# Performance work log

Measured on AMD Instinct MI355X. Metric: run time of the kernel, lower is better.

The kernel has to match this reference:

```python
import jax, jax.numpy as jnp
import numpy as np

M, NQ, NKV = 8, 256, 4096
E, H, D = 1024, 16, 64  # embed_dim, num_heads, head_dim
SCALE = D ** -0.5


def setup_inputs() -> dict:
    key = jax.random.key(0)
    ks = jax.random.split(key, 6)
    zq = jax.random.normal(ks[0], (M, NQ, E), dtype=jnp.float32)
    zkv = jax.random.normal(ks[1], (M, NKV, E), dtype=jnp.float32)
    xq = jax.random.normal(ks[2], (M, NQ, E), dtype=jnp.float32)
    xkv = jax.random.normal(ks[3], (M, NKV, E), dtype=jnp.float32)
    Wq = jax.random.normal(ks[4], (E, H * D), dtype=jnp.float32) / np.sqrt(E)
    Wk = jax.random.normal(ks[5], (E, H * D), dtype=jnp.float32) / np.sqrt(E)
    raw_head_weights = jnp.ones((H,), dtype=jnp.float32)
    return {"zq": zq, "zkv": zkv, "xq": xq, "xkv": xkv,
            "Wq": Wq, "Wk": Wk, "raw_head_weights": raw_head_weights}


def reference(zq, zkv, xq, xkv, Wq, Wk, raw_head_weights):
    # project + split heads: [m, h, n, d]
    q = jnp.einsum('mne,ehd->mhnd', zq, Wq.reshape(E, H, D))
    k = jnp.einsum('mne,ehd->mhnd', zkv, Wk.reshape(E, H, D))
    # SDPA with V = xkv broadcast across heads
    scores = jnp.einsum('mhqd,mhkd->mhqk', q, k) * SCALE
    attn = jax.nn.softmax(scores, axis=-1)
    # attn @ V with broadcast V [m, nkv, dx] -> per-head outputs [m, h, nq, dx]
    out = jnp.einsum('mhqk,mkd->mhqd', attn, xkv)
    # head-weighted combine + residual
    head_weights = jax.nn.softmax(raw_head_weights, axis=0)
    xq_update = jnp.einsum('mhqd,h->mqd', out, head_weights)
    xq_out = xq + xq_update
    return (zq, xq_out)
```

## Files before the change

### kernel.cpp

```cpp
#include <hip/hip_runtime.h>
#include <hip/hip_bf16.h>
#include <stdint.h>

#define MB_  8
#define NQ_  256
#define NKV_ 4096
#define E_   1024
#define H_   16
#define D_   64

typedef __bf16 bf16x8 __attribute__((ext_vector_type(8)));
typedef float  f32x4  __attribute__((ext_vector_type(4)));
typedef unsigned short u16;
typedef unsigned short u16x8 __attribute__((ext_vector_type(8)));

#define MFMA16(a,b,c) __builtin_amdgcn_mfma_f32_16x16x32_bf16((a),(b),(c),0,0,0)

__device__ __forceinline__ u16 f2bf(float f) {
  uint32_t u = __float_as_uint(f);
  u += 0x7fffu + ((u >> 16) & 1u);
  return (u16)(u >> 16);
}

__device__ __forceinline__ u16x8 pack8(f32x4 a, f32x4 b) {
  u16x8 v;
  v[0] = f2bf(a[0]); v[1] = f2bf(a[1]); v[2] = f2bf(a[2]); v[3] = f2bf(a[3]);
  v[4] = f2bf(b[0]); v[5] = f2bf(b[1]); v[6] = f2bf(b[2]); v[7] = f2bf(b[3]);
  return v;
}

__device__ __forceinline__ void gload_lds16(const void* g, void* l) {
  __builtin_amdgcn_global_load_lds(
      (const __attribute__((address_space(1))) void*)g,
      (__attribute__((address_space(3))) void*)l, 16, 0, 0);
}

__device__ __forceinline__ void stage_tile(const char* __restrict__ g, int ldbytes,
                                           char* lds, int t) {
  int srcCB = (((t & 7) ^ ((t >> 3) & 7)) << 4);
  const char* gp = g + (long long)(t >> 3) * ldbytes + srcCB;
  char* lp = lds + ((t >> 6) << 10);
#pragma unroll
  for (int i = 0; i < 4; ++i) {
    gload_lds16(gp + (long long)(32 * i) * ldbytes, lp + i * 4096);
  }
}

__device__ __forceinline__ bf16x8 read_frag(const char* lds, int r, int cb) {
  return *(const bf16x8*)(lds + r * 128 + (cb ^ ((r & 7) << 4)));
}

template <int MODE>
__global__ __launch_bounds__(256, 2) void gemm_nt(
    const u16* __restrict__ A, const u16* __restrict__ Bt, void* __restrict__ Cv,
    int lda, int ldb, int ldc, int K,
    long long sA, long long sB, long long sC) {
  __shared__ __align__(16) char smA[16384];
  __shared__ __align__(16) char smB[16384];
  int zz = blockIdx.z;
  int b = (MODE == 2) ? (zz & 7) : zz;
  int ks = (MODE == 2) ? (zz >> 3) : 0;
  long long koff = (long long)ks * 1024;

  unsigned nwg = gridDim.x * gridDim.y;
  unsigned orig = blockIdx.y * gridDim.x + blockIdx.x;
  unsigned cpx = nwg >> 3;
  unsigned swz = (orig & 7) * cpx + (orig >> 3);
  unsigned bx = swz % gridDim.x, by = swz / gridDim.x;

  const char* Ap = (const char*)(A + (long long)b * sA + (long long)by * 128 * lda + koff);
  const char* Bp = (const char*)(Bt + (long long)b * sB + (long long)bx * 128 * ldb + koff);

  int t = threadIdx.x, lane = t & 63;
  int wm = t >> 7, wn = (t >> 6) & 1;
  int rl = lane & 15, kq = lane >> 4;

  f32x4 acc[4][4];
#pragma unroll
  for (int i = 0; i < 4; ++i)
#pragma unroll
    for (int j = 0; j < 4; ++j) acc[i][j] = (f32x4){0.f, 0.f, 0.f, 0.f};

  int ldab = lda * 2, ldbb = ldb * 2;
  for (int k0 = 0; k0 < K; k0 += 64) {
    stage_tile(Ap + k0 * 2, ldab, smA, t);
    stage_tile(Bp + k0 * 2, ldbb, smB, t);
    __syncthreads();
    bf16x8 af[4][2], bf[4][2];
#pragma unroll
    for (int f = 0; f < 4; ++f)
#pragma unroll
      for (int ksl = 0; ksl < 2; ++ksl) {
        af[f][ksl] = read_frag(smA, wm * 64 + f * 16 + rl, ksl * 64 + kq * 16);
        bf[f][ksl] = read_frag(smB, wn * 64 + f * 16 + rl, ksl * 64 + kq * 16);
      }
#pragma unroll
    for (int fm = 0; fm < 4; ++fm)
#pragma unroll
      for (int fn = 0; fn < 4; ++fn) {
        acc[fm][fn] = MFMA16(af[fm][0], bf[fn][0], acc[fm][fn]);
        acc[fm][fn] = MFMA16(af[fm][1], bf[fn][1], acc[fm][fn]);
      }
    __syncthreads();
  }

#pragma unroll
  for (int fm = 0; fm < 4; ++fm)
#pragma unroll
    for (int fn = 0; fn < 4; ++fn)
#pragma unroll
      for (int j = 0; j < 4; ++j) {
        int row = by * 128 + wm * 64 + fm * 16 + kq * 4 + j;
        int col = bx * 128 + wn * 64 + fn * 16 + rl;
        if (MODE == 0) {
          ((u16*)Cv)[(long long)b * sC + (long long)row * ldc + col] = f2bf(acc[fm][fn][j]);
        } else {
          float* dst = (float*)Cv + ((long long)(ks * 8 + b)) * sC +
                       (long long)row * ldc + col;
          __builtin_nontemporal_store(acc[fm][fn][j], dst);
        }
      }
}

__device__ __forceinline__ void stage32(const char* __restrict__ g, int ldbytes,
                                        char* ldsbuf, int t, long long koffB) {
  int w = t >> 6, lane = t & 63;
#pragma unroll
  for (int i = 0; i < 2; ++i) {
    int c = w + i * 8;
    int slot = c * 64 + lane;
    int row = slot >> 2, c16 = slot & 3;
    int srcc = (c16 ^ ((row >> 1) & 3)) << 4;
    gload_lds16(g + (long long)row * ldbytes + koffB + srcc,
                ldsbuf + c * 1024);
  }
}

__device__ __forceinline__ bf16x8 frag32(const char* ldsbuf, int r, int kq) {
  return *(const bf16x8*)(ldsbuf + r * 64 + ((kq ^ ((r >> 1) & 3)) << 4));
}

__global__ __launch_bounds__(512, 2) void gemm256(
    const u16* __restrict__ A, const u16* __restrict__ Bt, u16* __restrict__ C,
    int lda, int ldb, int ldc, int K) {
  extern __shared__ char lds[];

  unsigned nwg = gridDim.x * gridDim.y;
  unsigned orig = blockIdx.y * gridDim.x + blockIdx.x;
  unsigned cpx = nwg >> 3;
  unsigned swz = (orig & 7) * cpx + (orig >> 3);
  unsigned bx = swz % gridDim.x, by = swz / gridDim.x;

  const char* Ap = (const char*)(A + (long long)by * 256 * lda);
  const char* Bp = (const char*)(Bt + (long long)bx * 256 * ldb);
  int ldab = lda * 2, ldbb = ldb * 2;

  int t = threadIdx.x, lane = t & 63;
  int wid = t >> 6, wm = wid >> 2, wn = wid & 3;
  int rl = lane & 15, kq = lane >> 4;

  f32x4 acc[8][4];
#pragma unroll
  for (int i = 0; i < 8; ++i)
#pragma unroll
    for (int j = 0; j < 4; ++j) acc[i][j] = (f32x4){0.f, 0.f, 0.f, 0.f};

  stage32(Ap, ldab, lds, t, 0);
  stage32(Bp, ldbb, lds + 16384, t, 0);
  stage32(Ap, ldab, lds + 32768, t, 64);
  stage32(Bp, ldbb, lds + 32768 + 16384, t, 64);
  asm volatile("s_waitcnt vmcnt(4)" ::: "memory");
  asm volatile("s_barrier" ::: "memory");

  int NT = K >> 5;
  for (int ts = 0; ts < NT; ++ts) {
    char* bufA = lds + (ts & 3) * 32768;
    char* bufB = bufA + 16384;
    if (ts + 2 < NT) {
      char* nb = lds + ((ts + 2) & 3) * 32768;
      stage32(Ap, ldab, nb, t, (long long)(ts + 2) << 6);
      stage32(Bp, ldbb, nb + 16384, t, (long long)(ts + 2) << 6);
    }
    bf16x8 af[8], bv[4];
#pragma unroll
    for (int fr = 0; fr < 8; ++fr) af[fr] = frag32(bufA, wm * 128 + fr * 16 + rl, kq);
#pragma unroll
    for (int fc = 0; fc < 4; ++fc) bv[fc] = frag32(bufB, wn * 64 + fc * 16 + rl, kq);
    __builtin_amdgcn_s_setprio(1);
#pragma unroll
    for (int fr = 0; fr < 8; ++fr)
#pragma unroll
      for (int fc = 0; fc < 4; ++fc)
        acc[fr][fc] = MFMA16(af[fr], bv[fc], acc[fr][fc]);
    __builtin_amdgcn_s_setprio(0);
    if (ts + 2 < NT)
      asm volatile("s_waitcnt vmcnt(4)" ::: "memory");
    else
      asm volatile("s_waitcnt vmcnt(0)" ::: "memory");
    asm volatile("s_barrier" ::: "memory");
  }

#pragma unroll
  for (int fr = 0; fr < 8; ++fr)
#pragma unroll
    for (int fc = 0; fc < 4; ++fc)
#pragma unroll
      for (int j = 0; j < 4; ++j) {
        int row = by * 256 + wm * 128 + fr * 16 + kq * 4 + j;
        int col = bx * 256 + wn * 64 + fc * 16 + rl;
        C[(long long)row * ldc + col] = f2bf(acc[fr][fc][j]);
      }
}

__global__ void pv_combine(const float* __restrict__ part, const float* __restrict__ xq,
                           float* __restrict__ out1) {
  int i = blockIdx.x * 256 + threadIdx.x;
  f32x4 s = __builtin_nontemporal_load((const f32x4*)xq + i);
#pragma unroll
  for (int k = 0; k < 4; ++k) {
    f32x4 p = __builtin_nontemporal_load((const f32x4*)(part + (long long)k * 2097152) + i);
    s += p;
  }
  ((f32x4*)out1)[i] = s;
}

__global__ __launch_bounds__(256, 4) void attn_stats(
    const u16* __restrict__ qg, const u16* __restrict__ kg,
    float* __restrict__ lstP) {
  __shared__ __align__(16) char smQ[16384];
  __shared__ __align__(16) char smK[16384];
  int kt = blockIdx.x, qt = blockIdx.y;
  int m = blockIdx.z >> 1, hh = blockIdx.z & 1;
  int t = threadIdx.x, lane = t & 63;
  int wm = t >> 7, wn = (t >> 6) & 1;
  int rl = lane & 15, kq = lane >> 4;

  const char* qbase = (const char*)(qg + ((long long)(m * NQ_ + qt * 128)) * 1024);
  const char* kbase = (const char*)(kg + ((long long)(m * NKV_ + kt * 128)) * 1024);

  for (int hi = 0; hi < 8; ++hi) {
    int h = hh * 8 + hi;
    stage_tile(qbase + h * 128, 2048, smQ, t);
    stage_tile(kbase + h * 128, 2048, smK, t);
    __syncthreads();
    bf16x8 kf[4][2], qf[4][2];
#pragma unroll
    for (int f = 0; f < 4; ++f)
#pragma unroll
      for (int ksl = 0; ksl < 2; ++ksl) {
        kf[f][ksl] = read_frag(smK, wm * 64 + f * 16 + rl, ksl * 64 + kq * 16);
        qf[f][ksl] = read_frag(smQ, wn * 64 + f * 16 + rl, ksl * 64 + kq * 16);
      }
    float rs[4] = {0.f, 0.f, 0.f, 0.f};
#pragma unroll
    for (int fm = 0; fm < 4; ++fm)
#pragma unroll
      for (int fn = 0; fn < 4; ++fn) {
        f32x4 sc = (f32x4){0.f, 0.f, 0.f, 0.f};
        sc = MFMA16(kf[fm][0], qf[fn][0], sc);
        sc = MFMA16(kf[fm][1], qf[fn][1], sc);
        rs[fn] += (__expf(sc[0]) + __expf(sc[1])) + (__expf(sc[2]) + __expf(sc[3]));
      }
#pragma unroll
    for (int fn = 0; fn < 4; ++fn) {
      float v = rs[fn];
      v += __shfl_xor(v, 16);
      v += __shfl_xor(v, 32);
      if (lane < 16) {
        int q = qt * 128 + wn * 64 + fn * 16 + rl;
        lstP[(long long)(kt * 2 + wm) * 32768 + ((m * H_ + h) << 8) + q] = v;
      }
    }
    __syncthreads();
  }
}

__global__ void stats_combine(const float* __restrict__ lp, float* __restrict__ lst) {
  int i = blockIdx.x * 256 + threadIdx.x;
  float s = 0.f;
#pragma unroll
  for (int k = 0; k < 64; ++k) s += lp[(long long)k * 32768 + i];
  lst[i] = s;
}

__global__ __launch_bounds__(256, 2) void pbar_kernel(
    const u16* __restrict__ qg, const u16* __restrict__ kg,
    const float* __restrict__ lstat,
    const float* __restrict__ rawhw, u16* __restrict__ Pbar) {
  __shared__ __align__(16) char smQ[16384];
  __shared__ __align__(16) char smK[16384];
  __shared__ float scf[2048];
  int kt = blockIdx.x, qt = blockIdx.y, m = blockIdx.z;
  int q0 = qt * 128, k0 = kt * 128;
  int t = threadIdx.x, lane = t & 63;
  int wm = t >> 7, wn = (t >> 6) & 1;
  int rl = lane & 15, kq = lane >> 4;

  float hm = -1e30f;
  for (int i = 0; i < H_; ++i) hm = fmaxf(hm, rawhw[i]);
  float hs = 0.f, hw[H_];
  for (int i = 0; i < H_; ++i) { hw[i] = __expf(rawhw[i] - hm); hs += hw[i]; }
  float hinv = 1.f / hs;
  for (int idx = t; idx < 2048; idx += 256) {
    int h = idx >> 7, r = idx & 127;
    scf[idx] = hw[h] * hinv / lstat[((m * H_ + h) << 8) + q0 + r];
  }

  f32x4 pacc[4][4];
#pragma unroll
  for (int i = 0; i < 4; ++i)
#pragma unroll
    for (int j = 0; j < 4; ++j) pacc[i][j] = (f32x4){0.f, 0.f, 0.f, 0.f};

  const char* qbase = (const char*)(qg + ((long long)(m * NQ_ + q0)) * 1024);
  const char* kbase = (const char*)(kg + ((long long)(m * NKV_ + k0)) * 1024);

  for (int h = 0; h < H_; ++h) {
    stage_tile(qbase + h * 128, 2048, smQ, t);
    stage_tile(kbase + h * 128, 2048, smK, t);
    __syncthreads();
    bf16x8 af[4][2], bfr[4][2];
#pragma unroll
    for (int f = 0; f < 4; ++f)
#pragma unroll
      for (int ksl = 0; ksl < 2; ++ksl) {
        af[f][ksl] = read_frag(smQ, wm * 64 + f * 16 + rl, ksl * 64 + kq * 16);
        bfr[f][ksl] = read_frag(smK, wn * 64 + f * 16 + rl, ksl * 64 + kq * 16);
      }
#pragma unroll
    for (int fm = 0; fm < 4; ++fm) {
      int rbase = wm * 64 + fm * 16 + kq * 4;
      float cf0 = scf[(h << 7) + rbase + 0];
      float cf1 = scf[(h << 7) + rbase + 1];
      float cf2 = scf[(h << 7) + rbase + 2];
      float cf3 = scf[(h << 7) + rbase + 3];
#pragma unroll
      for (int fn = 0; fn < 4; ++fn) {
        f32x4 sc = (f32x4){0.f, 0.f, 0.f, 0.f};
        sc = MFMA16(af[fm][0], bfr[fn][0], sc);
        sc = MFMA16(af[fm][1], bfr[fn][1], sc);
        pacc[fm][fn][0] += cf0 * __expf(sc[0]);
        pacc[fm][fn][1] += cf1 * __expf(sc[1]);
        pacc[fm][fn][2] += cf2 * __expf(sc[2]);
        pacc[fm][fn][3] += cf3 * __expf(sc[3]);
      }
    }
    __syncthreads();
  }
#pragma unroll
  for (int fm = 0; fm < 4; ++fm)
#pragma unroll
    for (int fn = 0; fn < 4; ++fn)
#pragma unroll
      for (int j = 0; j < 4; ++j) {
        int row = q0 + wm * 64 + fm * 16 + kq * 4 + j;
        int col = k0 + wn * 64 + fn * 16 + rl;
        Pbar[(((long long)m * NQ_ + row) << 12) + col] = f2bf(pacc[fm][fn][j]);
      }
}

__global__ void prep_kernel(const float* __restrict__ zq, u16* __restrict__ zqb,
                            float* __restrict__ out0,
                            const float* __restrict__ zkv, u16* __restrict__ zkvb,
                            const float* __restrict__ Wq, u16* __restrict__ WqT,
                            const float* __restrict__ Wk, u16* __restrict__ WkT,
                            const float* __restrict__ xkv, u16* __restrict__ xkvT) {
  __shared__ float tile[64][65];
  int bid = blockIdx.x;
  if (bid < 8704) {
    const float* in; u16* out; bool passthru; long long i;
    if (bid < 512) { in = zq; out = zqb; passthru = true; i = (long long)bid * 256 + threadIdx.x; }
    else { in = zkv; out = zkvb; passthru = false; i = (long long)(bid - 512) * 256 + threadIdx.x; }
    const f32x4* p = (const f32x4*)(in + i * 16);
    f32x4 a = __builtin_nontemporal_load(p);
    f32x4 b = __builtin_nontemporal_load(p + 1);
    f32x4 c = __builtin_nontemporal_load(p + 2);
    f32x4 d = __builtin_nontemporal_load(p + 3);
    if (passthru) {
      f32x4* o = (f32x4*)(out0 + i * 16);
      __builtin_nontemporal_store(a, o);
      __builtin_nontemporal_store(b, o + 1);
      __builtin_nontemporal_store(c, o + 2);
      __builtin_nontemporal_store(d, o + 3);
    }
    u16x8* q = (u16x8*)(out + i * 16);
    q[0] = pack8(a, b);
    q[1] = pack8(c, d);
    return;
  }
  const float* in; u16* out; int R, C; float alpha; int r0, c0; bool nts = false;
  if (bid < 8960) {
    int id = bid - 8704;
    in = Wq; out = WqT; R = 1024; C = 1024; alpha = 0.125f;
    r0 = (id & 15) * 64; c0 = (id >> 4) * 64;
  } else if (bid < 9216) {
    int id = bid - 8960;
    in = Wk; out = WkT; R = 1024; C = 1024; alpha = 1.0f;
    r0 = (id & 15) * 64; c0 = (id >> 4) * 64;
  } else {
    int id = bid - 9216;
    int bz = id >> 10, rem = id & 1023;
    in = xkv + (long long)bz * NKV_ * E_;
    out = xkvT + (long long)bz * NKV_ * E_;
    R = NKV_; C = E_; alpha = 1.0f;
    r0 = (rem & 63) * 64; c0 = (rem >> 6) * 64;
    nts = true;
  }
  int t = threadIdx.x;
  int rr = t >> 4, c4 = t & 15;
#pragma unroll
  for (int i = 0; i < 4; ++i) {
    f32x4 v = __builtin_nontemporal_load(
        (const f32x4*)(in + (long long)(r0 + rr + i * 16) * C + c0 + c4 * 4));
    float* d = &tile[rr + i * 16][c4 * 4];
    d[0] = v[0]; d[1] = v[1]; d[2] = v[2]; d[3] = v[3];
  }
  __syncthreads();
  int cc = t >> 3, r8 = t & 7;
#pragma unroll
  for (int i = 0; i < 2; ++i) {
    int c = cc + i * 32;
    u16x8 v;
#pragma unroll
    for (int j = 0; j < 8; ++j) v[j] = f2bf(alpha * tile[r8 * 8 + j][c]);
    u16x8* dst = (u16x8*)(out + (long long)(c0 + c) * R + r0 + r8 * 8);
    if (nts) __builtin_nontemporal_store(v, dst);
    else *dst = v;
  }
}

extern "C" void kernel_launch(void* const* d_in, const int* in_sizes, int n_in,
                              void* d_out, int out_size, void* d_ws, size_t ws_size,
                              hipStream_t stream) {
  const float* zq  = (const float*)d_in[0];
  const float* zkv = (const float*)d_in[1];
  const float* xq  = (const float*)d_in[2];
  const float* xkv = (const float*)d_in[3];
  const float* Wq  = (const float*)d_in[4];
  const float* Wk  = (const float*)d_in[5];
  const float* rhw = (const float*)d_in[6];
  float* out = (float*)d_out;

  char* ws = (char*)d_ws;
  u16* WqT  = (u16*)(ws);
  u16* WkT  = (u16*)(ws + (2ull << 20));
  u16* zqb  = (u16*)(ws + (4ull << 20));
  u16* qb   = (u16*)(ws + (8ull << 20));
  u16* kb   = (u16*)(ws + (12ull << 20));
  u16* xkvT = (u16*)(ws + (76ull << 20));
  char* zr  = ws + (140ull << 20);
  u16* zkvb = (u16*)zr;
  u16* Pbar = (u16*)zr;
  float* lst  = (float*)(zr + (18ull << 20));
  float* lstP = (float*)(zr + (20ull << 20));
  float* pvP  = (float*)(zr + (28ull << 20));

  (void)hipFuncSetAttribute((const void*)gemm256,
                            hipFuncAttributeMaxDynamicSharedMemorySize, 131072);

  prep_kernel<<<17408, 256, 0, stream>>>(zq, zqb, out, zkv, zkvb,
                                         Wq, WqT, Wk, WkT, xkv, xkvT);

  gemm_nt<0><<<dim3(8, 16, 1), 256, 0, stream>>>(zqb, WqT, qb,
                                                 1024, 1024, 1024, 1024, 0, 0, 0);
  gemm256<<<dim3(4, 128, 1), 512, 131072, stream>>>(zkvb, WkT, kb, 1024, 1024, 1024, 1024);

  attn_stats<<<dim3(32, 2, 16), 256, 0, stream>>>(qb, kb, lstP);
  stats_combine<<<128, 256, 0, stream>>>(lstP, lst);

  pbar_kernel<<<dim3(32, 2, 8), 256, 0, stream>>>(qb, kb, lst, rhw, Pbar);

  gemm_nt<2><<<dim3(8, 2, 32), 256, 0, stream>>>(Pbar, xkvT, pvP,
                                                 4096, 4096, 1024, 1024,
                                                 256LL * 4096, 1024LL * 4096,
                                                 256LL * 1024);
  pv_combine<<<2048, 256, 0, stream>>>(pvP, xq, out + (long long)MB_ * NQ_ * E_);
}
```

Before: 297.5 us.

## Double-buffer Q/K tiles in stats and Pbar kernels; fold log2e into Wq scale

attn_stats and pbar_kernel now ping-pong between two LDS buffers. Each iteration issues the direct-to-LDS loads for the next head before computing on the current one, with explicit vmcnt waits and raw s_barrier in place of __syncthreads. Separately, log2(e) is folded into the Wq prescale so the kernels can call exp2f instead of __expf, removing a multiply per exponential. The cost is twice the LDS (attn_stats launch bounds drop from 4 to 2 blocks per SM), and the hand-counted vmcnt values must match the number of loads stage_tile issues.

```diff
diff --git a/kernel.cpp b/kernel.cpp
--- a/kernel.cpp
+++ b/kernel.cpp
@@ -131,8 +131,7 @@
     int slot = c * 64 + lane;
     int row = slot >> 2, c16 = slot & 3;
     int srcc = (c16 ^ ((row >> 1) & 3)) << 4;
-    gload_lds16(g + (long long)row * ldbytes + koffB + srcc,
-                ldsbuf + c * 1024);
+    gload_lds16(g + (long long)row * ldbytes + koffB + srcc, ldsbuf + c * 1024);
   }
 }
 
@@ -224,32 +223,43 @@
   ((f32x4*)out1)[i] = s;
 }
 
-__global__ __launch_bounds__(256, 4) void attn_stats(
+__global__ __launch_bounds__(256, 2) void attn_stats(
     const u16* __restrict__ qg, const u16* __restrict__ kg,
     float* __restrict__ lstP) {
-  __shared__ __align__(16) char smQ[16384];
-  __shared__ __align__(16) char smK[16384];
+  __shared__ __align__(16) char sm[2][32768];
   int kt = blockIdx.x, qt = blockIdx.y;
   int m = blockIdx.z >> 1, hh = blockIdx.z & 1;
   int t = threadIdx.x, lane = t & 63;
   int wm = t >> 7, wn = (t >> 6) & 1;
   int rl = lane & 15, kq = lane >> 4;
 
-  const char* qbase = (const char*)(qg + ((long long)(m * NQ_ + qt * 128)) * 1024);
-  const char* kbase = (const char*)(kg + ((long long)(m * NKV_ + kt * 128)) * 1024);
+  const char* qbase = (const char*)(qg + ((long long)(m * NQ_ + qt * 128)) * 1024)
+                      + (long long)hh * 8 * 128;
+  const char* kbase = (const char*)(kg + ((long long)(m * NKV_ + kt * 128)) * 1024)
+                      + (long long)hh * 8 * 128;
+
+  stage_tile(qbase, 2048, sm[0], t);
+  stage_tile(kbase, 2048, sm[0] + 16384, t);
 
   for (int hi = 0; hi < 8; ++hi) {
-    int h = hh * 8 + hi;
-    stage_tile(qbase + h * 128, 2048, smQ, t);
-    stage_tile(kbase + h * 128, 2048, smK, t);
-    __syncthreads();
+    const char* cur = sm[hi & 1];
+    if (hi + 1 < 8) {
+      char* nxt = sm[(hi + 1) & 1];
+      stage_tile(qbase + (hi + 1) * 128, 2048, nxt, t);
+      stage_tile(kbase + (hi + 1) * 128, 2048, nxt + 16384, t);
+      asm volatile("s_waitcnt vmcnt(8)" ::: "memory");
+    } else {
+      asm volatile("s_waitcnt vmcnt(0)" ::: "memory");
+    }
+    asm volatile("s_barrier" ::: "memory");
+
     bf16x8 kf[4][2], qf[4][2];
 #pragma unroll
     for (int f = 0; f < 4; ++f)
 #pragma unroll
       for (int ksl = 0; ksl < 2; ++ksl) {
-        kf[f][ksl] = read_frag(smK, wm * 64 + f * 16 + rl, ksl * 64 + kq * 16);
-        qf[f][ksl] = read_frag(smQ, wn * 64 + f * 16 + rl, ksl * 64 + kq * 16);
+        kf[f][ksl] = read_frag(cur + 16384, wm * 64 + f * 16 + rl, ksl * 64 + kq * 16);
+        qf[f][ksl] = read_frag(cur, wn * 64 + f * 16 + rl, ksl * 64 + kq * 16);
       }
     float rs[4] = {0.f, 0.f, 0.f, 0.f};
 #pragma unroll
@@ -259,7 +269,7 @@
         f32x4 sc = (f32x4){0.f, 0.f, 0.f, 0.f};
         sc = MFMA16(kf[fm][0], qf[fn][0], sc);
         sc = MFMA16(kf[fm][1], qf[fn][1], sc);
-        rs[fn] += (__expf(sc[0]) + __expf(sc[1])) + (__expf(sc[2]) + __expf(sc[3]));
+        rs[fn] += (exp2f(sc[0]) + exp2f(sc[1])) + (exp2f(sc[2]) + exp2f(sc[3]));
       }
 #pragma unroll
     for (int fn = 0; fn < 4; ++fn) {
@@ -267,11 +277,12 @@
       v += __shfl_xor(v, 16);
       v += __shfl_xor(v, 32);
       if (lane < 16) {
+        int h = hh * 8 + hi;
         int q = qt * 128 + wn * 64 + fn * 16 + rl;
         lstP[(long long)(kt * 2 + wm) * 32768 + ((m * H_ + h) << 8) + q] = v;
       }
     }
-    __syncthreads();
+    asm volatile("s_barrier" ::: "memory");
   }
 }
 
@@ -287,14 +298,19 @@
     const u16* __restrict__ qg, const u16* __restrict__ kg,
     const float* __restrict__ lstat,
     const float* __restrict__ rawhw, u16* __restrict__ Pbar) {
-  __shared__ __align__(16) char smQ[16384];
-  __shared__ __align__(16) char smK[16384];
+  __shared__ __align__(16) char sm[2][32768];
   __shared__ float scf[2048];
   int kt = blockIdx.x, qt = blockIdx.y, m = blockIdx.z;
   int q0 = qt * 128, k0 = kt * 128;
   int t = threadIdx.x, lane = t & 63;
   int wm = t >> 7, wn = (t >> 6) & 1;
   int rl = lane & 15, kq = lane >> 4;
+
+  const char* qbase = (const char*)(qg + ((long long)(m * NQ_ + q0)) * 1024);
+  const char* kbase = (const char*)(kg + ((long long)(m * NKV_ + k0)) * 1024);
+
+  stage_tile(qbase, 2048, sm[0], t);
+  stage_tile(kbase, 2048, sm[0] + 16384, t);
 
   float hm = -1e30f;
   for (int i = 0; i < H_; ++i) hm = fmaxf(hm, rawhw[i]);
@@ -305,6 +321,7 @@
     int h = idx >> 7, r = idx & 127;
     scf[idx] = hw[h] * hinv / lstat[((m * H_ + h) << 8) + q0 + r];
   }
+  asm volatile("s_waitcnt lgkmcnt(0)" ::: "memory");
 
   f32x4 pacc[4][4];
 #pragma unroll
@@ -312,20 +329,25 @@
 #pragma unroll
     for (int j = 0; j < 4; ++j) pacc[i][j] = (f32x4){0.f, 0.f, 0.f, 0.f};
 
-  const char* qbase = (const char*)(qg + ((long long)(m * NQ_ + q0)) * 1024);
-  const char* kbase = (const char*)(kg + ((long long)(m * NKV_ + k0)) * 1024);
-
   for (int h = 0; h < H_; ++h) {
-    stage_tile(qbase + h * 128, 2048, smQ, t);
-    stage_tile(kbase + h * 128, 2048, smK, t);
-    __syncthreads();
+    const char* cur = sm[h & 1];
+    if (h + 1 < H_) {
+      char* nxt = sm[(h + 1) & 1];
+      stage_tile(qbase + (h + 1) * 128, 2048, nxt, t);
+      stage_tile(kbase + (h + 1) * 128, 2048, nxt + 16384, t);
+      asm volatile("s_waitcnt vmcnt(8)" ::: "memory");
+    } else {
+      asm volatile("s_waitcnt vmcnt(0)" ::: "memory");
+    }
+    asm volatile("s_barrier" ::: "memory");
+
     bf16x8 af[4][2], bfr[4][2];
 #pragma unroll
     for (int f = 0; f < 4; ++f)
 #pragma unroll
       for (int ksl = 0; ksl < 2; ++ksl) {
-        af[f][ksl] = read_frag(smQ, wm * 64 + f * 16 + rl, ksl * 64 + kq * 16);
-        bfr[f][ksl] = read_frag(smK, wn * 64 + f * 16 + rl, ksl * 64 + kq * 16);
+        af[f][ksl] = read_frag(cur, wm * 64 + f * 16 + rl, ksl * 64 + kq * 16);
+        bfr[f][ksl] = read_frag(cur + 16384, wn * 64 + f * 16 + rl, ksl * 64 + kq * 16);
       }
 #pragma unroll
     for (int fm = 0; fm < 4; ++fm) {
@@ -339,13 +361,13 @@
         f32x4 sc = (f32x4){0.f, 0.f, 0.f, 0.f};
         sc = MFMA16(af[fm][0], bfr[fn][0], sc);
         sc = MFMA16(af[fm][1], bfr[fn][1], sc);
-        pacc[fm][fn][0] += cf0 * __expf(sc[0]);
-        pacc[fm][fn][1] += cf1 * __expf(sc[1]);
-        pacc[fm][fn][2] += cf2 * __expf(sc[2]);
-        pacc[fm][fn][3] += cf3 * __expf(sc[3]);
+        pacc[fm][fn][0] += cf0 * exp2f(sc[0]);
+        pacc[fm][fn][1] += cf1 * exp2f(sc[1]);
+        pacc[fm][fn][2] += cf2 * exp2f(sc[2]);
+        pacc[fm][fn][3] += cf3 * exp2f(sc[3]);
       }
     }
-    __syncthreads();
+    asm volatile("s_barrier" ::: "memory");
   }
 #pragma unroll
   for (int fm = 0; fm < 4; ++fm)
@@ -391,7 +413,8 @@
   const float* in; u16* out; int R, C; float alpha; int r0, c0; bool nts = false;
   if (bid < 8960) {
     int id = bid - 8704;
-    in = Wq; out = WqT; R = 1024; C = 1024; alpha = 0.125f;
+    in = Wq; out = WqT; R = 1024; C = 1024;
+    alpha = 0.125f * 1.44269504088896f;
     r0 = (id & 15) * 64; c0 = (id >> 4) * 64;
   } else if (bid < 9216) {
     int id = bid - 8960;
```

Result: slower. 326.2 us (+9.7%).
